# Kernel optimization log

Measured on AMD Instinct MI355X. Metric: run time of the kernel, lower is better.

## Reference

```python
import jax, jax.numpy as jnp
import numpy as np

H = 2048   # hidden_size
K = 2048   # key_size
Q = 2048   # query_size
S = 8192   # source sequence length
V = 2048   # value feature dim


def setup_inputs() -> dict:
    key = jax.random.key(0)
    ks = jax.random.split(key, 6)
    query = jax.random.normal(ks[0], (1, 1, Q), dtype=jnp.float32)
    src_key = jax.random.normal(ks[1], (1, S, K), dtype=jnp.float32)
    values = jax.random.normal(ks[2], (S, V), dtype=jnp.float32)
    # nn.Linear weights are [out, in]; all bias-free
    Wq = jax.random.normal(ks[3], (H, Q), dtype=jnp.float32) / np.sqrt(Q)
    Wk = jax.random.normal(ks[4], (H, K), dtype=jnp.float32) / np.sqrt(K)
    Ws = jax.random.normal(ks[5], (1, H), dtype=jnp.float32) / np.sqrt(H)
    return {"query": query, "key": src_key, "values": values,
            "Wq": Wq, "Wk": Wk, "Ws": Ws}


def reference(query, key, values, Wq, Wk, Ws):
    # projected_query: [1,1,H]; projected_key: [1,S,H]
    pq = jnp.einsum('btq,hq->bth', query, Wq)
    pk = jnp.einsum('bsk,hk->bsh', key, Wk)
    # additive (Bahdanau) scores: [1,S,1] -> squeeze(2).unsqueeze(1) -> [1,1,S]
    scores = jnp.einsum('bsh,oh->bso', jnp.tanh(pq + pk), Ws)
    scores = scores[:, :, 0][:, None, :]
    attention_weights = jax.nn.softmax(scores, axis=-1)        # [1,1,S]
    # bmm([1,1,S], values.unsqueeze(0)=[1,S,V]) -> [1,1,V]
    context = jnp.einsum('bts,sv->btv', attention_weights, values)
    return (attention_weights, context)
```

## Files before the change

### kernel.cpp

```cpp
#include <hip/hip_runtime.h>
#include <hip/hip_bf16.h>
#include <math.h>

#define HDIM 2048
#define KDIM 2048
#define SDIM 8192
#define VDIM 2048
#define BKT  64
#define NT   (KDIM / BKT)

using short8 = __attribute__((ext_vector_type(8))) short;
using f32x4  = __attribute__((ext_vector_type(4))) float;
using us8    = __attribute__((ext_vector_type(8))) unsigned short;

typedef const __attribute__((address_space(1))) void g_void;
typedef __attribute__((address_space(3))) void lds_void;

__device__ __forceinline__ unsigned short f2bf(float f) {
  union { float f; unsigned int u; } x; x.f = f;
  unsigned int r = x.u + 0x7fffu + ((x.u >> 16) & 1u);
  return (unsigned short)(r >> 16);
}

__device__ __forceinline__ float tanh_fast(float x) {
  float e = __expf(2.0f * x);
  return 1.0f - 2.0f * __builtin_amdgcn_rcpf(e + 1.0f);
}

__device__ __forceinline__ void barrier_sync() {
  asm volatile("" ::: "memory");
  __builtin_amdgcn_s_barrier();
  asm volatile("" ::: "memory");
}

__global__ __launch_bounds__(256) void cvt_kernel(const float* __restrict__ in,
                                                  unsigned short* __restrict__ out,
                                                  int n8) {
  int i = blockIdx.x * 256 + threadIdx.x;
  if (i >= n8) return;
  f32x4 a = *(const f32x4*)&in[(size_t)i * 8];
  f32x4 b = *(const f32x4*)&in[(size_t)i * 8 + 4];
  us8 o;
  #pragma unroll
  for (int j = 0; j < 4; ++j) { o[j] = f2bf(a[j]); o[j + 4] = f2bf(b[j]); }
  *(us8*)&out[(size_t)i * 8] = o;
}

__global__ __launch_bounds__(256) void pq_kernel(const float* __restrict__ query,
                                                 const float* __restrict__ Wq,
                                                 float* __restrict__ pq) {
  int wave = threadIdx.x >> 6, lane = threadIdx.x & 63;
  int h = blockIdx.x * 4 + wave;
  const float* w = Wq + (size_t)h * KDIM;
  float s = 0.f;
  for (int i = lane; i < KDIM; i += 64) s = fmaf(query[i], w[i], s);
  #pragma unroll
  for (int off = 32; off; off >>= 1) s += __shfl_xor(s, off);
  if (lane == 0) pq[h] = s;
}

__global__ __launch_bounds__(512, 2) void scores_kernel(const unsigned short* __restrict__ keybf,
                                                        const unsigned short* __restrict__ wkbf,
                                                        const float* __restrict__ pq,
                                                        const float* __restrict__ Ws,
                                                        float* __restrict__ partial) {
  __shared__ unsigned short lds[65536];

  const int tid = threadIdx.x;
  const int bid = blockIdx.x;
  const int xg = bid & 7, xi = bid >> 3;
  const int bx = xg * 4 + (xi & 3);
  const int by = xi >> 2;
  const int s0 = bx * 256, h0 = by * 256;

  const int wave = tid >> 6, lane = tid & 63;
  const int wm = wave >> 2, wn = wave & 3;
  const int l16 = lane & 15, g16 = lane >> 4;

  const int srow = tid >> 3;
  const int scol = ((tid & 7) * 16) ^ ((srow & 7) << 4);
  const char* aSrc0 = (const char*)keybf + ((size_t)(s0 + srow) * KDIM) * 2 + scol;
  const char* bSrc0 = (const char*)wkbf  + ((size_t)(h0 + srow) * KDIM) * 2 + scol;

  #define STAGE_A(o, kt, buf) __builtin_amdgcn_global_load_lds( \
      (g_void*)(aSrc0 + (size_t)(o) * 64 * KDIM * 2 + (size_t)(kt) * 128), \
      (lds_void*)((char*)lds + (size_t)(buf) * 65536 + (o) * 8192 + wave * 1024), 16, 0, 0)
  #define STAGE_B(o, kt, buf) __builtin_amdgcn_global_load_lds( \
      (g_void*)(bSrc0 + (size_t)(o) * 64 * KDIM * 2 + (size_t)(kt) * 128), \
      (lds_void*)((char*)lds + (size_t)(buf) * 65536 + 32768 + (o) * 8192 + wave * 1024), 16, 0, 0)

  const int xorv = (l16 & 7) << 4;
  int colx[2];
  colx[0] = ((g16 * 16)      ) ^ xorv;
  colx[1] = ((g16 * 16) | 64 ) ^ xorv;
  const int aRowBase = (wm * 128 + l16) * 128;
  const int bRowBase = 32768 + (wn * 64 + l16) * 128;

  f32x4 acc[8][4];
  #pragma unroll
  for (int m = 0; m < 8; ++m)
    #pragma unroll
    for (int n = 0; n < 4; ++n) acc[m][n] = (f32x4)(0.0f);

  #pragma unroll
  for (int o = 0; o < 4; ++o) STAGE_A(o, 0, 0);
  #pragma unroll
  for (int o = 0; o < 4; ++o) STAGE_B(o, 0, 0);
  asm volatile("s_waitcnt vmcnt(0)" ::: "memory");
  barrier_sync();

  short8 af[4][2], bf_[4][2];

  for (int t = 0; t < NT; ++t) {
    const int cbase = (t & 1) * 65536;
    const int nbuf = (t & 1) ^ 1;
    const bool more = (t + 1 < NT);

    #pragma unroll
    for (int m = 0; m < 4; ++m)
      #pragma unroll
      for (int ks = 0; ks < 2; ++ks)
        af[m][ks] = *(const short8*)((const char*)lds + cbase + aRowBase + m * 2048 + colx[ks]);
    #pragma unroll
    for (int n = 0; n < 2; ++n)
      #pragma unroll
      for (int ks = 0; ks < 2; ++ks)
        bf_[n][ks] = *(const short8*)((const char*)lds + cbase + bRowBase + n * 2048 + colx[ks]);
    if (more) {
      STAGE_A(0, t + 1, nbuf); STAGE_A(1, t + 1, nbuf);
      STAGE_A(2, t + 1, nbuf); STAGE_A(3, t + 1, nbuf);
    }
    barrier_sync();
    __builtin_amdgcn_s_setprio(1);
    #pragma unroll
    for (int m = 0; m < 4; ++m)
      #pragma unroll
      for (int n = 0; n < 2; ++n)
        #pragma unroll
        for (int ks = 0; ks < 2; ++ks)
          acc[m][n] = __builtin_amdgcn_mfma_f32_16x16x32_bf16(af[m][ks], bf_[n][ks], acc[m][n], 0, 0, 0);
    __builtin_amdgcn_s_setprio(0);
    barrier_sync();

    #pragma unroll
    for (int n = 2; n < 4; ++n)
      #pragma unroll
      for (int ks = 0; ks < 2; ++ks)
        bf_[n][ks] = *(const short8*)((const char*)lds + cbase + bRowBase + n * 2048 + colx[ks]);
    if (more) {
      STAGE_B(0, t + 1, nbuf); STAGE_B(1, t + 1, nbuf);
      STAGE_B(2, t + 1, nbuf); STAGE_B(3, t + 1, nbuf);
    }
    barrier_sync();
    __builtin_amdgcn_s_setprio(1);
    #pragma unroll
    for (int m = 0; m < 4; ++m)
      #pragma unroll
      for (int n = 2; n < 4; ++n)
        #pragma unroll
        for (int ks = 0; ks < 2; ++ks)
          acc[m][n] = __builtin_amdgcn_mfma_f32_16x16x32_bf16(af[m][ks], bf_[n][ks], acc[m][n], 0, 0, 0);
    __builtin_amdgcn_s_setprio(0);
    barrier_sync();

    #pragma unroll
    for (int m = 0; m < 4; ++m)
      #pragma unroll
      for (int ks = 0; ks < 2; ++ks)
        af[m][ks] = *(const short8*)((const char*)lds + cbase + aRowBase + (m + 4) * 2048 + colx[ks]);
    barrier_sync();
    __builtin_amdgcn_s_setprio(1);
    #pragma unroll
    for (int m = 0; m < 4; ++m)
      #pragma unroll
      for (int n = 2; n < 4; ++n)
        #pragma unroll
        for (int ks = 0; ks < 2; ++ks)
          acc[m + 4][n] = __builtin_amdgcn_mfma_f32_16x16x32_bf16(af[m][ks], bf_[n][ks], acc[m + 4][n], 0, 0, 0);
    __builtin_amdgcn_s_setprio(0);
    barrier_sync();

    __builtin_amdgcn_s_setprio(1);
    #pragma unroll
    for (int m = 0; m < 4; ++m)
      #pragma unroll
      for (int n = 0; n < 2; ++n)
        #pragma unroll
        for (int ks = 0; ks < 2; ++ks)
          acc[m + 4][n] = __builtin_amdgcn_mfma_f32_16x16x32_bf16(af[m][ks], bf_[n][ks], acc[m + 4][n], 0, 0, 0);
    __builtin_amdgcn_s_setprio(0);
    asm volatile("s_waitcnt vmcnt(0)" ::: "memory");
    barrier_sync();
  }

  float pqv[4], wsv[4];
  #pragma unroll
  for (int n = 0; n < 4; ++n) {
    int h = h0 + wn * 64 + n * 16 + l16;
    pqv[n] = pq[h];
    wsv[n] = Ws[h];
  }

  float* sred = (float*)lds;
  #pragma unroll
  for (int m = 0; m < 8; ++m) {
    #pragma unroll
    for (int j = 0; j < 4; ++j) {
      float rs = 0.f;
      #pragma unroll
      for (int n = 0; n < 4; ++n)
        rs += tanh_fast(acc[m][n][j] + pqv[n]) * wsv[n];
      rs += __shfl_xor(rs, 1);
      rs += __shfl_xor(rs, 2);
      rs += __shfl_xor(rs, 4);
      rs += __shfl_xor(rs, 8);
      if (l16 == 0)
        sred[(wm * 128 + m * 16 + g16 * 4 + j) * 4 + wn] = rs;
    }
  }
  __syncthreads();
  if (tid < 256) {
    float v = sred[tid * 4 + 0] + sred[tid * 4 + 1] + sred[tid * 4 + 2] + sred[tid * 4 + 3];
    partial[(size_t)(s0 + tid) * 8 + by] = v;
  }
}

__global__ __launch_bounds__(1024) void softmax_kernel(const float* __restrict__ partial,
                                                       float* __restrict__ weights) {
  __shared__ float red[16];
  int tid = threadIdx.x;
  int sbase = tid * 8;
  float sc[8];
  float mx = -1e30f;
  #pragma unroll
  for (int i = 0; i < 8; ++i) {
    const float* p = partial + (size_t)(sbase + i) * 8;
    float v = 0.f;
    #pragma unroll
    for (int q = 0; q < 8; ++q) v += p[q];
    sc[i] = v;
    mx = fmaxf(mx, v);
  }
  #pragma unroll
  for (int off = 32; off; off >>= 1) mx = fmaxf(mx, __shfl_xor(mx, off));
  if ((tid & 63) == 0) red[tid >> 6] = mx;
  __syncthreads();
  float gmx = red[0];
  #pragma unroll
  for (int q = 1; q < 16; ++q) gmx = fmaxf(gmx, red[q]);
  __syncthreads();
  float ls = 0.f;
  #pragma unroll
  for (int i = 0; i < 8; ++i) { sc[i] = expf(sc[i] - gmx); ls += sc[i]; }
  #pragma unroll
  for (int off = 32; off; off >>= 1) ls += __shfl_xor(ls, off);
  if ((tid & 63) == 0) red[tid >> 6] = ls;
  __syncthreads();
  float gs = 0.f;
  #pragma unroll
  for (int q = 0; q < 16; ++q) gs += red[q];
  float inv = 1.0f / gs;
  #pragma unroll
  for (int i = 0; i < 8; ++i) weights[sbase + i] = sc[i] * inv;
}

__global__ __launch_bounds__(256) void ctx_partial_kernel(const float* __restrict__ values,
                                                          const float* __restrict__ w,
                                                          float* __restrict__ part) {
  int vcol4 = blockIdx.x * 256 + threadIdx.x;
  int ss0 = blockIdx.y * 128;
  f32x4 acc = (f32x4)(0.0f);
  for (int s = ss0; s < ss0 + 128; ++s) {
    f32x4 v = *(const f32x4*)&values[(size_t)s * VDIM + vcol4 * 4];
    float ws = w[s];
    #pragma unroll
    for (int j = 0; j < 4; ++j) acc[j] = fmaf(ws, v[j], acc[j]);
  }
  *(f32x4*)&part[(size_t)blockIdx.y * VDIM + vcol4 * 4] = acc;
}

__global__ __launch_bounds__(256) void ctx_reduce_kernel(const float* __restrict__ part,
                                                         float* __restrict__ ctx) {
  int vcol = blockIdx.x * 256 + threadIdx.x;
  float acc = 0.f;
  #pragma unroll
  for (int p = 0; p < 64; ++p) acc += part[(size_t)p * VDIM + vcol];
  ctx[vcol] = acc;
}

extern "C" void kernel_launch(void* const* d_in, const int* in_sizes, int n_in,
                              void* d_out, int out_size, void* d_ws, size_t ws_size,
                              hipStream_t stream) {
  const float* query  = (const float*)d_in[0];
  const float* key    = (const float*)d_in[1];
  const float* values = (const float*)d_in[2];
  const float* Wq     = (const float*)d_in[3];
  const float* Wk     = (const float*)d_in[4];
  const float* Ws     = (const float*)d_in[5];

  float* out     = (float*)d_out;
  float* weights = out;
  float* ctx     = out + SDIM;

  char* ws = (char*)d_ws;
  unsigned short* keybf = (unsigned short*)ws;
  unsigned short* wkbf  = (unsigned short*)(ws + (size_t)SDIM * KDIM * 2);
  char* tail = ws + (size_t)SDIM * KDIM * 2 + (size_t)HDIM * KDIM * 2;
  float* pq      = (float*)tail;
  float* partial = (float*)(tail + 8192);
  float* cpart   = (float*)(tail + 8192 + (size_t)SDIM * 8 * 4);

  cvt_kernel<<<(SDIM * KDIM / 8 + 255) / 256, 256, 0, stream>>>(key, keybf, SDIM * KDIM / 8);
  cvt_kernel<<<(HDIM * KDIM / 8 + 255) / 256, 256, 0, stream>>>(Wk, wkbf, HDIM * KDIM / 8);
  pq_kernel<<<HDIM / 4, 256, 0, stream>>>(query, Wq, pq);
  scores_kernel<<<256, 512, 0, stream>>>(keybf, wkbf, pq, Ws, partial);
  softmax_kernel<<<1, 1024, 0, stream>>>(partial, weights);
  ctx_partial_kernel<<<dim3(VDIM / (256 * 4), 64), 256, 0, stream>>>(values, weights, cpart);
  ctx_reduce_kernel<<<VDIM / 256, 256, 0, stream>>>(cpart, ctx);
}
```

Before: 131.7 us.

## Spread GEMM prefetch across phases, fuse conversions, vectorize pq, split ctx finer

The scores GEMM main loop now issues next-tile LDS prefetches in smaller groups across the four compute phases. It uses partial vmcnt waits instead of one full drain at the end of each iteration, so global loads overlap more of the MFMA work. The two fp32-to-bf16 conversion launches are merged into one kernel, the pq matvec is vectorized to float4 loads, and the context reduction uses twice as many S-chunks to raise parallelism. The partial waits depend on exact load ordering into buffers that are still being read, which raises the risk of race conditions. The ctx partial buffer doubles in size, which may overflow the workspace layout.

```diff
diff --git a/kernel.cpp b/kernel.cpp
--- a/kernel.cpp
+++ b/kernel.cpp
@@ -33,17 +33,19 @@
   asm volatile("" ::: "memory");
 }
 
-__global__ __launch_bounds__(256) void cvt_kernel(const float* __restrict__ in,
-                                                  unsigned short* __restrict__ out,
-                                                  int n8) {
+__global__ __launch_bounds__(256) void cvt_kernel(const float* __restrict__ key,
+                                                  const float* __restrict__ Wk,
+                                                  unsigned short* __restrict__ outbf,
+                                                  int keyN8, int totN8) {
   int i = blockIdx.x * 256 + threadIdx.x;
-  if (i >= n8) return;
-  f32x4 a = *(const f32x4*)&in[(size_t)i * 8];
-  f32x4 b = *(const f32x4*)&in[(size_t)i * 8 + 4];
+  if (i >= totN8) return;
+  const float* src = (i < keyN8) ? &key[(size_t)i * 8] : &Wk[((size_t)i - keyN8) * 8];
+  f32x4 a = *(const f32x4*)src;
+  f32x4 b = *(const f32x4*)(src + 4);
   us8 o;
   #pragma unroll
   for (int j = 0; j < 4; ++j) { o[j] = f2bf(a[j]); o[j + 4] = f2bf(b[j]); }
-  *(us8*)&out[(size_t)i * 8] = o;
+  *(us8*)&outbf[(size_t)i * 8] = o;
 }
 
 __global__ __launch_bounds__(256) void pq_kernel(const float* __restrict__ query,
@@ -52,8 +54,15 @@
   int wave = threadIdx.x >> 6, lane = threadIdx.x & 63;
   int h = blockIdx.x * 4 + wave;
   const float* w = Wq + (size_t)h * KDIM;
-  float s = 0.f;
-  for (int i = lane; i < KDIM; i += 64) s = fmaf(query[i], w[i], s);
+  f32x4 s4 = (f32x4)(0.0f);
+  #pragma unroll
+  for (int i = 0; i < KDIM / 256; ++i) {
+    f32x4 q4 = *(const f32x4*)&query[lane * 4 + i * 256];
+    f32x4 w4 = *(const f32x4*)&w[lane * 4 + i * 256];
+    #pragma unroll
+    for (int j = 0; j < 4; ++j) s4[j] = fmaf(q4[j], w4[j], s4[j]);
+  }
+  float s = s4[0] + s4[1] + s4[2] + s4[3];
   #pragma unroll
   for (int off = 32; off; off >>= 1) s += __shfl_xor(s, off);
   if (lane == 0) pq[h] = s;
@@ -102,11 +111,10 @@
     #pragma unroll
     for (int n = 0; n < 4; ++n) acc[m][n] = (f32x4)(0.0f);
 
-  #pragma unroll
-  for (int o = 0; o < 4; ++o) STAGE_A(o, 0, 0);
-  #pragma unroll
-  for (int o = 0; o < 4; ++o) STAGE_B(o, 0, 0);
-  asm volatile("s_waitcnt vmcnt(0)" ::: "memory");
+  STAGE_A(0, 0, 0); STAGE_A(2, 0, 0);
+  STAGE_B(0, 0, 0); STAGE_B(1, 0, 0); STAGE_B(2, 0, 0); STAGE_B(3, 0, 0);
+  STAGE_A(1, 0, 0); STAGE_A(3, 0, 0);
+  asm volatile("s_waitcnt vmcnt(2)" ::: "memory");
   barrier_sync();
 
   short8 af[4][2], bf_[4][2];
@@ -126,10 +134,7 @@
       #pragma unroll
       for (int ks = 0; ks < 2; ++ks)
         bf_[n][ks] = *(const short8*)((const char*)lds + cbase + bRowBase + n * 2048 + colx[ks]);
-    if (more) {
-      STAGE_A(0, t + 1, nbuf); STAGE_A(1, t + 1, nbuf);
-      STAGE_A(2, t + 1, nbuf); STAGE_A(3, t + 1, nbuf);
-    }
+    if (more) { STAGE_A(0, t + 1, nbuf); STAGE_A(2, t + 1, nbuf); }
     barrier_sync();
     __builtin_amdgcn_s_setprio(1);
     #pragma unroll
@@ -149,7 +154,9 @@
         bf_[n][ks] = *(const short8*)((const char*)lds + cbase + bRowBase + n * 2048 + colx[ks]);
     if (more) {
       STAGE_B(0, t + 1, nbuf); STAGE_B(1, t + 1, nbuf);
-      STAGE_B(2, t + 1, nbuf); STAGE_B(3, t + 1, nbuf);
+      asm volatile("s_waitcnt vmcnt(4)" ::: "memory");
+    } else {
+      asm volatile("s_waitcnt vmcnt(0)" ::: "memory");
     }
     barrier_sync();
     __builtin_amdgcn_s_setprio(1);
@@ -168,6 +175,7 @@
       #pragma unroll
       for (int ks = 0; ks < 2; ++ks)
         af[m][ks] = *(const short8*)((const char*)lds + cbase + aRowBase + (m + 4) * 2048 + colx[ks]);
+    if (more) { STAGE_B(2, t + 1, nbuf); STAGE_B(3, t + 1, nbuf); }
     barrier_sync();
     __builtin_amdgcn_s_setprio(1);
     #pragma unroll
@@ -180,6 +188,7 @@
     __builtin_amdgcn_s_setprio(0);
     barrier_sync();
 
+    if (more) { STAGE_A(1, t + 1, nbuf); STAGE_A(3, t + 1, nbuf); }
     __builtin_amdgcn_s_setprio(1);
     #pragma unroll
     for (int m = 0; m < 4; ++m)
@@ -189,7 +198,8 @@
         for (int ks = 0; ks < 2; ++ks)
           acc[m + 4][n] = __builtin_amdgcn_mfma_f32_16x16x32_bf16(af[m][ks], bf_[n][ks], acc[m + 4][n], 0, 0, 0);
     __builtin_amdgcn_s_setprio(0);
-    asm volatile("s_waitcnt vmcnt(0)" ::: "memory");
+    if (more)
+      asm volatile("s_waitcnt vmcnt(2)" ::: "memory");
     barrier_sync();
   }
 
@@ -268,9 +278,9 @@
                                                           const float* __restrict__ w,
                                                           float* __restrict__ part) {
   int vcol4 = blockIdx.x * 256 + threadIdx.x;
-  int ss0 = blockIdx.y * 128;
+  int ss0 = blockIdx.y * 64;
   f32x4 acc = (f32x4)(0.0f);
-  for (int s = ss0; s < ss0 + 128; ++s) {
+  for (int s = ss0; s < ss0 + 64; ++s) {
     f32x4 v = *(const f32x4*)&values[(size_t)s * VDIM + vcol4 * 4];
     float ws = w[s];
     #pragma unroll
@@ -284,7 +294,7 @@
   int vcol = blockIdx.x * 256 + threadIdx.x;
   float acc = 0.f;
   #pragma unroll
-  for (int p = 0; p < 64; ++p) acc += part[(size_t)p * VDIM + vcol];
+  for (int p = 0; p < 128; ++p) acc += part[(size_t)p * VDIM + vcol];
   ctx[vcol] = acc;
 }
 
@@ -310,11 +320,12 @@
   float* partial = (float*)(tail + 8192);
   float* cpart   = (float*)(tail + 8192 + (size_t)SDIM * 8 * 4);
 
-  cvt_kernel<<<(SDIM * KDIM / 8 + 255) / 256, 256, 0, stream>>>(key, keybf, SDIM * KDIM / 8);
-  cvt_kernel<<<(HDIM * KDIM / 8 + 255) / 256, 256, 0, stream>>>(Wk, wkbf, HDIM * KDIM / 8);
+  const int keyN8 = SDIM * KDIM / 8;
+  const int totN8 = keyN8 + HDIM * KDIM / 8;
+  cvt_kernel<<<(totN8 + 255) / 256, 256, 0, stream>>>(key, Wk, keybf, keyN8, totN8);
   pq_kernel<<<HDIM / 4, 256, 0, stream>>>(query, Wq, pq);
   scores_kernel<<<256, 512, 0, stream>>>(keybf, wkbf, pq, Ws, partial);
   softmax_kernel<<<1, 1024, 0, stream>>>(partial, weights);
-  ctx_partial_kernel<<<dim3(VDIM / (256 * 4), 64), 256, 0, stream>>>(values, weights, cpart);
+  ctx_partial_kernel<<<dim3(VDIM / (256 * 4), 128), 256, 0, stream>>>(values, weights, cpart);
   ctx_reduce_kernel<<<VDIM / 256, 256, 0, stream>>>(cpart, ctx);
 }
```

Result: slower. 137.7 us (+4.5%).
